# Performance work log

Measured on AMD Instinct MI355X. Metric: run time of the kernel, lower is better.

## Reference

```python
import jax, jax.numpy as jnp
import numpy as np

N = 50000
E = 400000
IN_FEATS = 256
HIDDEN = 64
HEADS = 8
CLASSES = 40
NEG_SLOPE = 0.2  # DGL GATConv default negative_slope


def setup_inputs() -> dict:
    key = jax.random.key(0)
    ks = jax.random.split(key, 12)
    features = jax.random.normal(ks[0], (N, IN_FEATS), dtype=jnp.float32)
    src = jax.random.randint(ks[1], (E,), 0, N, dtype=jnp.int32)
    dst = jax.random.randint(ks[2], (E,), 0, N, dtype=jnp.int32)
    s = 0.05
    # layer 0: in_feats -> HEADS*HIDDEN
    W1 = jax.random.normal(ks[3], (IN_FEATS, HEADS * HIDDEN), dtype=jnp.float32) * s
    al1 = jax.random.normal(ks[4], (HEADS, HIDDEN), dtype=jnp.float32) * s
    ar1 = jax.random.normal(ks[5], (HEADS, HIDDEN), dtype=jnp.float32) * s
    # layer 1: HEADS*HIDDEN -> HEADS*HIDDEN
    W2 = jax.random.normal(ks[6], (HEADS * HIDDEN, HEADS * HIDDEN), dtype=jnp.float32) * s
    al2 = jax.random.normal(ks[7], (HEADS, HIDDEN), dtype=jnp.float32) * s
    ar2 = jax.random.normal(ks[8], (HEADS, HIDDEN), dtype=jnp.float32) * s
    # layer 2: HEADS*HIDDEN -> 1*CLASSES
    W3 = jax.random.normal(ks[9], (HEADS * HIDDEN, CLASSES), dtype=jnp.float32) * s
    al3 = jax.random.normal(ks[10], (1, CLASSES), dtype=jnp.float32) * s
    ar3 = jax.random.normal(ks[11], (1, CLASSES), dtype=jnp.float32) * s
    return {"features": features, "src": src, "dst": dst,
            "W1": W1, "al1": al1, "ar1": ar1,
            "W2": W2, "al2": al2, "ar2": ar2,
            "W3": W3, "al3": al3, "ar3": ar3}


def gat_conv(h, W, al, ar, src, dst):
    """DGL GATConv (no bias, no residual, no activation, no dropout)."""
    H, D = al.shape
    feat = (h @ W).reshape(N, H, D)                      # [N,H,D]
    el = jnp.sum(feat * al[None], axis=-1)               # [N,H]
    er = jnp.sum(feat * ar[None], axis=-1)               # [N,H]
    e = jax.nn.leaky_relu(el[src] + er[dst], NEG_SLOPE)  # [E,H]
    # edge softmax over incoming edges of each dst node
    m = jax.ops.segment_max(e, dst, num_segments=N)      # [N,H]
    ex = jnp.exp(e - m[dst])                             # [E,H]
    denom = jax.ops.segment_sum(ex, dst, num_segments=N) # [N,H]
    alpha = ex / denom[dst]                              # [E,H]
    msg = alpha[:, :, None] * feat[src]                  # [E,H,D]
    out = jax.ops.segment_sum(msg, dst, num_segments=N)  # [N,H,D]
    return out.reshape(N, H * D)


def reference(features, src, dst, W1, al1, ar1, W2, al2, ar2, W3, al3, ar3):
    h = gat_conv(features, W1, al1, ar1, src, dst)  # [N, HEADS*HIDDEN]
    h = gat_conv(h, W2, al2, ar2, src, dst)         # [N, HEADS*HIDDEN]
    h = gat_conv(h, W3, al3, ar3, src, dst)         # [N, CLASSES]
    return h
```

## Files before the change

### kernel.cpp

```cpp
#include <hip/hip_runtime.h>
#include <hip/hip_bf16.h>

#define NN 50000
#define NE 400000
#define MPAD 50048
#define SLOTS 48

typedef __bf16 bf16x8_t __attribute__((ext_vector_type(8)));
typedef __bf16 bf16x4_t __attribute__((ext_vector_type(4)));
typedef float f32x4_t __attribute__((ext_vector_type(4)));

__device__ __forceinline__ float bhi(unsigned int u) {
    union { unsigned int i; float f; } v; v.i = u & 0xffff0000u; return v.f;
}
__device__ __forceinline__ float blo(unsigned int u) {
    union { unsigned int i; float f; } v; v.i = u << 16; return v.f;
}

__global__ __launch_bounds__(256) void prep_kernel(
    const float* __restrict__ W1, __hip_bfloat16* __restrict__ W1t,
    const float* __restrict__ W2, __hip_bfloat16* __restrict__ W2t,
    const float* __restrict__ W3, __hip_bfloat16* __restrict__ W3t,
    const float* __restrict__ al1, const float* __restrict__ ar1,
    const float* __restrict__ al2, const float* __restrict__ ar2,
    __hip_bfloat16* __restrict__ walr1, __hip_bfloat16* __restrict__ walr2) {
    int stride = gridDim.x * blockDim.x;
    for (int i = blockIdx.x * blockDim.x + threadIdx.x; i < 512 * 512; i += stride) {
        if (i < 512 * 256) {
            int n = i >> 8, k = i & 255;
            W1t[i] = __float2bfloat16(W1[k * 512 + n]);
        }
        {
            int n = i >> 9, k = i & 511;
            W2t[i] = __float2bfloat16(W2[k * 512 + n]);
        }
        if (i < 48 * 512) {
            int n = i >> 9, k = i & 511;
            W3t[i] = __float2bfloat16((n < 40) ? W3[k * 40 + n] : 0.f);
        }
        if (i < 16 * 256) {
            int j = i >> 8, k = i & 255;
            const float* v = (j < 8) ? (al1 + j * 64) : (ar1 + (j - 8) * 64);
            float s = 0.f;
            for (int d = 0; d < 64; ++d) s += W1[(size_t)k * 512 + (j & 7) * 64 + d] * v[d];
            walr1[(k >> 5) * 512 + j * 32 + (k & 31)] = __float2bfloat16(s);
        }
        if (i < 16 * 512) {
            int j = i >> 9, k = i & 511;
            const float* v = (j < 8) ? (al2 + j * 64) : (ar2 + (j - 8) * 64);
            float s = 0.f;
            for (int d = 0; d < 64; ++d) s += W2[(size_t)k * 512 + (j & 7) * 64 + d] * v[d];
            walr2[(k >> 5) * 512 + j * 32 + (k & 31)] = __float2bfloat16(s);
        }
    }
}

__global__ void build_kernel(const int* __restrict__ src, const int* __restrict__ dst,
                             int* __restrict__ deg, int* __restrict__ slot) {
    int e = blockIdx.x * blockDim.x + threadIdx.x;
    if (e < NE) {
        int d = dst[e];
        int p = atomicAdd(&deg[d], 1);
        if (p < SLOTS) slot[(size_t)d * SLOTS + p] = src[e];
    }
}

__device__ __forceinline__ void gld_lds16(const void* g, void* l) {
    __builtin_amdgcn_global_load_lds(
        (const __attribute__((address_space(1))) unsigned int*)g,
        (__attribute__((address_space(3))) unsigned int*)l, 16, 0, 0);
}

__global__ __launch_bounds__(256) void gemm1_fused(const float* __restrict__ A,
                                                   const __hip_bfloat16* __restrict__ Wt,
                                                   const __hip_bfloat16* __restrict__ walr,
                                                   __hip_bfloat16* __restrict__ C,
                                                   float* __restrict__ el,
                                                   float* __restrict__ er) {
    const int K = 256;
    __shared__ __align__(16) char smem[16384];
    char* smemA = smem;
    char* smemB = smem + 8192;
    const int row0 = blockIdx.x * 128;
    const int col0 = blockIdx.y * 128;
    const int w = threadIdx.x >> 6;
    const int lane = threadIdx.x & 63;
    const int quad = lane >> 4, l15 = lane & 15;
    const int wm = (w >> 1) * 64, wn = (w & 1) * 64;
    const int c0 = w * 2;
    const int srow = lane >> 2;
    const int skel = (lane & 3) * 8;
    const bool my_e = (blockIdx.y == 0) && ((w & 1) == 0);

    f32x4_t acc[4][4] = {};
    f32x4_t acce[4] = {};
    for (int k0 = 0; k0 < K; k0 += 32) {
        __syncthreads();
        {
#pragma unroll
            for (int cc = 0; cc < 2; ++cc) {
                int row = row0 + (c0 + cc) * 16 + srow;
                int rc = (row < NN) ? row : (NN - 1);
                const float* p = A + (size_t)rc * K + k0 + skel;
                float4 f0 = *reinterpret_cast<const float4*>(p);
                float4 f1 = *reinterpret_cast<const float4*>(p + 4);
                bf16x8_t h;
                h[0] = (__bf16)f0.x; h[1] = (__bf16)f0.y;
                h[2] = (__bf16)f0.z; h[3] = (__bf16)f0.w;
                h[4] = (__bf16)f1.x; h[5] = (__bf16)f1.y;
                h[6] = (__bf16)f1.z; h[7] = (__bf16)f1.w;
                *reinterpret_cast<bf16x8_t*>(smemA + (c0 + cc) * 1024 + srow * 64 +
                                             (lane & 3) * 16) = h;
            }
            const __hip_bfloat16* gB0 = Wt + (size_t)(col0 + c0 * 16 + srow) * K + k0 + skel;
            gld_lds16(gB0, smemB + c0 * 1024);
            gld_lds16(gB0 + (size_t)16 * K, smemB + (c0 + 1) * 1024);
        }
        __syncthreads();
        bf16x8_t a[4], b[4];
#pragma unroll
        for (int mi = 0; mi < 4; mi++)
            a[mi] = *reinterpret_cast<const bf16x8_t*>(smemA + (wm + mi * 16 + l15) * 64 + quad * 16);
#pragma unroll
        for (int ni = 0; ni < 4; ni++)
            b[ni] = *reinterpret_cast<const bf16x8_t*>(smemB + (wn + ni * 16 + l15) * 64 + quad * 16);
#pragma unroll
        for (int mi = 0; mi < 4; mi++)
#pragma unroll
            for (int ni = 0; ni < 4; ni++)
                acc[mi][ni] = __builtin_amdgcn_mfma_f32_16x16x32_bf16(a[mi], b[ni], acc[mi][ni], 0, 0, 0);
        if (my_e) {
            bf16x8_t b5 = *reinterpret_cast<const bf16x8_t*>(
                walr + (k0 >> 5) * 512 + l15 * 32 + quad * 8);
#pragma unroll
            for (int mi = 0; mi < 4; mi++)
                acce[mi] = __builtin_amdgcn_mfma_f32_16x16x32_bf16(a[mi], b5, acce[mi], 0, 0, 0);
        }
    }
#pragma unroll
    for (int mi = 0; mi < 4; mi++) {
#pragma unroll
        for (int ni = 0; ni < 4; ni++) {
#pragma unroll
            for (int r = 0; r < 4; r++) {
                int row = row0 + wm + mi * 16 + quad * 4 + r;
                if (row < NN)
                    C[(size_t)row * 512 + col0 + wn + ni * 16 + l15] =
                        __float2bfloat16(acc[mi][ni][r]);
            }
        }
    }
    if (my_e) {
#pragma unroll
        for (int mi = 0; mi < 4; mi++) {
#pragma unroll
            for (int r = 0; r < 4; r++) {
                int row = row0 + wm + mi * 16 + quad * 4 + r;
                if (row < NN) {
                    float v = acce[mi][r];
                    if (l15 < 8) el[row * 8 + l15] = v;
                    else er[row * 8 + l15 - 8] = v;
                }
            }
        }
    }
}

__global__ __launch_bounds__(256) void gemm_bt_fused(const __hip_bfloat16* __restrict__ A,
                                                     const __hip_bfloat16* __restrict__ Wt,
                                                     const __hip_bfloat16* __restrict__ walr,
                                                     __hip_bfloat16* __restrict__ C,
                                                     float* __restrict__ el,
                                                     float* __restrict__ er) {
    const int K = 512;
    __shared__ __align__(16) char smem[16384];
    char* smemA = smem;
    char* smemB = smem + 8192;
    const int row0 = blockIdx.x * 128;
    const int col0 = blockIdx.y * 128;
    const int w = threadIdx.x >> 6;
    const int lane = threadIdx.x & 63;
    const int quad = lane >> 4, l15 = lane & 15;
    const int wm = (w >> 1) * 64, wn = (w & 1) * 64;
    const int c0 = w * 2;
    const int srow = lane >> 2;
    const int skel = (lane & 3) * 8;
    const bool my_e = (blockIdx.y == 0) && ((w & 1) == 0);

    f32x4_t acc[4][4] = {};
    f32x4_t acce[4] = {};
    for (int k0 = 0; k0 < K; k0 += 32) {
        __syncthreads();
        {
            const __hip_bfloat16* gA0 = A + (size_t)(row0 + c0 * 16 + srow) * K + k0 + skel;
            const __hip_bfloat16* gB0 = Wt + (size_t)(col0 + c0 * 16 + srow) * K + k0 + skel;
            gld_lds16(gA0, smemA + c0 * 1024);
            gld_lds16(gA0 + (size_t)16 * K, smemA + (c0 + 1) * 1024);
            gld_lds16(gB0, smemB + c0 * 1024);
            gld_lds16(gB0 + (size_t)16 * K, smemB + (c0 + 1) * 1024);
        }
        __syncthreads();
        bf16x8_t a[4], b[4];
#pragma unroll
        for (int mi = 0; mi < 4; mi++)
            a[mi] = *reinterpret_cast<const bf16x8_t*>(smemA + (wm + mi * 16 + l15) * 64 + quad * 16);
#pragma unroll
        for (int ni = 0; ni < 4; ni++)
            b[ni] = *reinterpret_cast<const bf16x8_t*>(smemB + (wn + ni * 16 + l15) * 64 + quad * 16);
#pragma unroll
        for (int mi = 0; mi < 4; mi++)
#pragma unroll
            for (int ni = 0; ni < 4; ni++)
                acc[mi][ni] = __builtin_amdgcn_mfma_f32_16x16x32_bf16(a[mi], b[ni], acc[mi][ni], 0, 0, 0);
        if (my_e) {
            bf16x8_t b5 = *reinterpret_cast<const bf16x8_t*>(
                walr + (k0 >> 5) * 512 + l15 * 32 + quad * 8);
#pragma unroll
            for (int mi = 0; mi < 4; mi++)
                acce[mi] = __builtin_amdgcn_mfma_f32_16x16x32_bf16(a[mi], b5, acce[mi], 0, 0, 0);
        }
    }
#pragma unroll
    for (int mi = 0; mi < 4; mi++) {
#pragma unroll
        for (int ni = 0; ni < 4; ni++) {
#pragma unroll
            for (int r = 0; r < 4; r++) {
                int row = row0 + wm + mi * 16 + quad * 4 + r;
                if (row < NN)
                    C[(size_t)row * 512 + col0 + wn + ni * 16 + l15] =
                        __float2bfloat16(acc[mi][ni][r]);
            }
        }
    }
    if (my_e) {
#pragma unroll
        for (int mi = 0; mi < 4; mi++) {
#pragma unroll
            for (int r = 0; r < 4; r++) {
                int row = row0 + wm + mi * 16 + quad * 4 + r;
                if (row < NN) {
                    float v = acce[mi][r];
                    if (l15 < 8) el[row * 8 + l15] = v;
                    else er[row * 8 + l15 - 8] = v;
                }
            }
        }
    }
}

#define W3_LDSROW 520
__global__ __launch_bounds__(256) void gemm3_mfma(const __hip_bfloat16* __restrict__ A,
                                                  const __hip_bfloat16* __restrict__ W3t,
                                                  const float* __restrict__ al,
                                                  const float* __restrict__ ar,
                                                  __hip_bfloat16* __restrict__ C,
                                                  float* __restrict__ el,
                                                  float* __restrict__ er) {
    __shared__ __align__(16) __hip_bfloat16 wlds[48 * W3_LDSROW];
    for (int c = threadIdx.x; c < 48 * 64; c += 256) {
        int n = c >> 6, koff = (c & 63) * 8;
        *reinterpret_cast<uint4*>(&wlds[n * W3_LDSROW + koff]) =
            *reinterpret_cast<const uint4*>(W3t + n * 512 + koff);
    }
    __syncthreads();
    const int w = threadIdx.x >> 6;
    const int lane = threadIdx.x & 63;
    const int quad = lane >> 4, l15 = lane & 15;
    const int row0 = blockIdx.x * 64 + w * 16;

    float alv[3], arv[3];
#pragma unroll
    for (int c = 0; c < 3; c++) {
        int col = c * 16 + l15;
        alv[c] = (col < 40) ? al[col] : 0.f;
        arv[c] = (col < 40) ? ar[col] : 0.f;
    }

    f32x4_t acc[3] = {};
    const __hip_bfloat16* arow = A + (size_t)(row0 + l15) * 512;
#pragma unroll 4
    for (int k0 = 0; k0 < 512; k0 += 32) {
        bf16x8_t a = *reinterpret_cast<const bf16x8_t*>(arow + k0 + quad * 8);
#pragma unroll
        for (int c = 0; c < 3; c++) {
            bf16x8_t b = *reinterpret_cast<const bf16x8_t*>(
                &wlds[(c * 16 + l15) * W3_LDSROW + k0 + quad * 8]);
            acc[c] = __builtin_amdgcn_mfma_f32_16x16x32_bf16(a, b, acc[c], 0, 0, 0);
        }
    }
#pragma unroll
    for (int r = 0; r < 4; r++) {
        int row = row0 + quad * 4 + r;
        bool rok = row < NN;
        float pl = 0.f, pr = 0.f;
#pragma unroll
        for (int c = 0; c < 3; c++) {
            float v = acc[c][r];
            if (rok) C[(size_t)row * 64 + c * 16 + l15] = __float2bfloat16(v);
            pl += v * alv[c];
            pr += v * arv[c];
        }
        if (rok) C[(size_t)row * 64 + 48 + l15] = __float2bfloat16(0.f);
        pl += __shfl_xor(pl, 1, 64); pr += __shfl_xor(pr, 1, 64);
        pl += __shfl_xor(pl, 2, 64); pr += __shfl_xor(pr, 2, 64);
        pl += __shfl_xor(pl, 4, 64); pr += __shfl_xor(pr, 4, 64);
        pl += __shfl_xor(pl, 8, 64); pr += __shfl_xor(pr, 8, 64);
        if (l15 == 0 && rok) { el[row] = pl; er[row] = pr; }
    }
}

__global__ __launch_bounds__(256) void agg8_kernel(const __hip_bfloat16* __restrict__ feat,
                                                   const float* __restrict__ el,
                                                   const float* __restrict__ er,
                                                   const int* __restrict__ deg,
                                                   const int* __restrict__ slot,
                                                   __hip_bfloat16* __restrict__ out) {
    int gw = (blockIdx.x * blockDim.x + threadIdx.x) >> 6;
    int n = gw >> 1, w = gw & 1;
    int lane = threadIdx.x & 63;
    if (n >= NN) return;
    const int es = lane >> 2;
    const int h4 = lane & 3;
    const int hd = lane >> 4;
    int dn = min(deg[n], SLOTS);
    float er_n = er[n * 8 + w * 4 + h4];
    const int* sl = slot + (size_t)n * SLOTS;

    float lsum = 0.f;
    float acc[4] = {};
    for (int base = 0; base < dn; base += 16) {
        int e = base + es;
        bool valid = e < dn;
        int s = valid ? sl[e] : 0;
        float t = el[s * 8 + w * 4 + h4] + er_n;
        float x = (t >= 0.f) ? t : 0.2f * t;
        float p = valid ? __expf(x) : 0.f;
        lsum += p;
        int cnt = min(16, dn - base);
        for (int j = 0; j < cnt; ++j) {
            int sj = __shfl(s, j * 4, 64);
            float pj = __shfl(p, j * 4 + hd, 64);
            uint2 q = *reinterpret_cast<const uint2*>(feat + (size_t)sj * 512 + w * 256 + lane * 4);
            acc[0] += pj * blo(q.x); acc[1] += pj * bhi(q.x);
            acc[2] += pj * blo(q.y); acc[3] += pj * bhi(q.y);
        }
    }
    lsum += __shfl_xor(lsum, 4, 64);
    lsum += __shfl_xor(lsum, 8, 64);
    lsum += __shfl_xor(lsum, 16, 64);
    lsum += __shfl_xor(lsum, 32, 64);
    float lh = __shfl(lsum, hd, 64);
    float inv = (lh > 0.f) ? 1.f / lh : 0.f;
    bf16x4_t o4;
#pragma unroll
    for (int d = 0; d < 4; ++d) o4[d] = (__bf16)(acc[d] * inv);
    *reinterpret_cast<bf16x4_t*>(out + (size_t)n * 512 + w * 256 + lane * 4) = o4;
}

__global__ __launch_bounds__(256) void agg3_kernel(const __hip_bfloat16* __restrict__ feat,
                                                   const float* __restrict__ el,
                                                   const float* __restrict__ er,
                                                   const int* __restrict__ deg,
                                                   const int* __restrict__ slot,
                                                   float* __restrict__ out) {
    int n = (blockIdx.x * blockDim.x + threadIdx.x) >> 6;
    int lane = threadIdx.x & 63;
    if (n >= NN) return;
    const int es = lane >> 3;
    const int dc = lane & 7;
    int dn = min(deg[n], SLOTS);
    float er_n = er[n];
    const int* sl = slot + (size_t)n * SLOTS;

    float lsum = 0.f;
    float acc[8] = {};
    for (int base = 0; base < dn; base += 16) {
        int e0 = base + es, e1 = base + 8 + es;
        bool v0 = e0 < dn, v1 = e1 < dn;
        int s0 = v0 ? sl[e0] : 0;
        int s1 = v1 ? sl[e1] : 0;
        float t0 = el[s0] + er_n;
        float t1 = el[s1] + er_n;
        float x0 = (t0 >= 0.f) ? t0 : 0.2f * t0;
        float x1 = (t1 >= 0.f) ? t1 : 0.2f * t1;
        float p0 = v0 ? __expf(x0) : 0.f;
        float p1 = v1 ? __expf(x1) : 0.f;
        lsum += p0 + p1;
        uint4 q0 = *reinterpret_cast<const uint4*>(feat + (size_t)s0 * 64 + dc * 8);
        uint4 q1 = *reinterpret_cast<const uint4*>(feat + (size_t)s1 * 64 + dc * 8);
        acc[0] += p0 * blo(q0.x) + p1 * blo(q1.x);
        acc[1] += p0 * bhi(q0.x) + p1 * bhi(q1.x);
        acc[2] += p0 * blo(q0.y) + p1 * blo(q1.y);
        acc[3] += p0 * bhi(q0.y) + p1 * bhi(q1.y);
        acc[4] += p0 * blo(q0.z) + p1 * blo(q1.z);
        acc[5] += p0 * bhi(q0.z) + p1 * bhi(q1.z);
        acc[6] += p0 * blo(q0.w) + p1 * blo(q1.w);
        acc[7] += p0 * bhi(q0.w) + p1 * bhi(q1.w);
    }
    lsum += __shfl_xor(lsum, 8, 64);
    lsum += __shfl_xor(lsum, 16, 64);
    lsum += __shfl_xor(lsum, 32, 64);
#pragma unroll
    for (int d = 0; d < 8; ++d) {
        acc[d] += __shfl_xor(acc[d], 8, 64);
        acc[d] += __shfl_xor(acc[d], 16, 64);
        acc[d] += __shfl_xor(acc[d], 32, 64);
    }
    float inv = (lsum > 0.f) ? 1.f / lsum : 0.f;
    if (es == 0 && dc < 5) {
        float4 o0 = make_float4(acc[0] * inv, acc[1] * inv, acc[2] * inv, acc[3] * inv);
        float4 o1 = make_float4(acc[4] * inv, acc[5] * inv, acc[6] * inv, acc[7] * inv);
        *reinterpret_cast<float4*>(out + (size_t)n * 40 + dc * 8) = o0;
        *reinterpret_cast<float4*>(out + (size_t)n * 40 + dc * 8 + 4) = o1;
    }
}

extern "C" void kernel_launch(void* const* d_in, const int* in_sizes, int n_in,
                              void* d_out, int out_size, void* d_ws, size_t ws_size,
                              hipStream_t stream) {
    const float* features = (const float*)d_in[0];
    const int* src = (const int*)d_in[1];
    const int* dst = (const int*)d_in[2];
    const float* W1 = (const float*)d_in[3];
    const float* al1 = (const float*)d_in[4];
    const float* ar1 = (const float*)d_in[5];
    const float* W2 = (const float*)d_in[6];
    const float* al2 = (const float*)d_in[7];
    const float* ar2 = (const float*)d_in[8];
    const float* W3 = (const float*)d_in[9];
    const float* al3 = (const float*)d_in[10];
    const float* ar3 = (const float*)d_in[11];

    char* ws = (char*)d_ws;
    size_t o = 0;
    auto carve = [&](size_t bytes) -> void* {
        o = (o + 255) & ~(size_t)255;
        void* p = ws + o;
        o += bytes;
        return p;
    };
    __hip_bfloat16* Fbf = (__hip_bfloat16*)carve((size_t)MPAD * 512 * 2);
    __hip_bfloat16* Gbf = (__hip_bfloat16*)carve((size_t)MPAD * 512 * 2);
    __hip_bfloat16* W1t = (__hip_bfloat16*)carve((size_t)512 * 256 * 2);
    __hip_bfloat16* W2t = (__hip_bfloat16*)carve((size_t)512 * 512 * 2);
    __hip_bfloat16* W3t = (__hip_bfloat16*)carve((size_t)48 * 512 * 2);
    __hip_bfloat16* walr1 = (__hip_bfloat16*)carve((size_t)16 * 256 * 2);
    __hip_bfloat16* walr2 = (__hip_bfloat16*)carve((size_t)16 * 512 * 2);
    float* el = (float*)carve((size_t)NN * 8 * 4);
    float* er = (float*)carve((size_t)NN * 8 * 4);
    float* el3 = (float*)carve((size_t)NN * 4);
    float* er3 = (float*)carve((size_t)NN * 4);
    int* deg = (int*)carve((size_t)NN * 4);
    int* slot = (int*)carve((size_t)NN * SLOTS * 4);

    hipMemsetAsync(deg, 0, (size_t)NN * 4, stream);
    build_kernel<<<(NE + 255) / 256, 256, 0, stream>>>(src, dst, deg, slot);
    prep_kernel<<<512, 256, 0, stream>>>(W1, W1t, W2, W2t, W3, W3t,
                                         al1, ar1, al2, ar2, walr1, walr2);

    const int gmm = MPAD / 128;
    gemm1_fused<<<dim3(gmm, 4), 256, 0, stream>>>(features, W1t, walr1, Fbf, el, er);
    agg8_kernel<<<(2 * NN + 3) / 4, 256, 0, stream>>>(Fbf, el, er, deg, slot, Gbf);
    gemm_bt_fused<<<dim3(gmm, 4), 256, 0, stream>>>(Gbf, W2t, walr2, Fbf, el, er);
    agg8_kernel<<<(2 * NN + 3) / 4, 256, 0, stream>>>(Fbf, el, er, deg, slot, Gbf);
    gemm3_mfma<<<MPAD / 64, 256, 0, stream>>>(Gbf, W3t, al3, ar3, Fbf, el3, er3);
    agg3_kernel<<<(NN + 3) / 4, 256, 0, stream>>>(Fbf, el3, er3, deg, slot, (float*)d_out);
}
```

Measured before the change: 440.6 us.

## Aggregate all 8 heads per wavefront with 16-byte gathers and 4-way unrolled edges

The 8-head aggregation kernel now gives each destination node a single wavefront covering all 512 features, instead of two wavefronts each covering half. Each lane loads 8 bf16 values (16 bytes) per source row and gets the source index through readlane. The edge loop is unrolled by four so several independent gathers are in flight at once. This halves the wavefront count and the redundant slot, el and exp work per node, at the cost of more registers per lane and fewer waves to hide latency.

```diff
diff --git a/kernel.cpp b/kernel.cpp
--- a/kernel.cpp
+++ b/kernel.cpp
@@ -310,52 +310,75 @@
     }
 }
 
+__device__ __forceinline__ void fma8(float* acc, float pj, const uint4& q) {
+    acc[0] += pj * blo(q.x); acc[1] += pj * bhi(q.x);
+    acc[2] += pj * blo(q.y); acc[3] += pj * bhi(q.y);
+    acc[4] += pj * blo(q.z); acc[5] += pj * bhi(q.z);
+    acc[6] += pj * blo(q.w); acc[7] += pj * bhi(q.w);
+}
+
 __global__ __launch_bounds__(256) void agg8_kernel(const __hip_bfloat16* __restrict__ feat,
                                                    const float* __restrict__ el,
                                                    const float* __restrict__ er,
                                                    const int* __restrict__ deg,
                                                    const int* __restrict__ slot,
                                                    __hip_bfloat16* __restrict__ out) {
-    int gw = (blockIdx.x * blockDim.x + threadIdx.x) >> 6;
-    int n = gw >> 1, w = gw & 1;
+    int n = (blockIdx.x * blockDim.x + threadIdx.x) >> 6;
     int lane = threadIdx.x & 63;
     if (n >= NN) return;
-    const int es = lane >> 2;
-    const int h4 = lane & 3;
-    const int hd = lane >> 4;
+    const int es = lane >> 3;
+    const int h8 = lane & 7;
+    const int hd = lane >> 3;
     int dn = min(deg[n], SLOTS);
-    float er_n = er[n * 8 + w * 4 + h4];
+    float er_n = er[n * 8 + h8];
     const int* sl = slot + (size_t)n * SLOTS;
 
     float lsum = 0.f;
-    float acc[4] = {};
-    for (int base = 0; base < dn; base += 16) {
+    float acc[8] = {};
+    for (int base = 0; base < dn; base += 8) {
         int e = base + es;
         bool valid = e < dn;
         int s = valid ? sl[e] : 0;
-        float t = el[s * 8 + w * 4 + h4] + er_n;
+        float t = el[s * 8 + h8] + er_n;
         float x = (t >= 0.f) ? t : 0.2f * t;
         float p = valid ? __expf(x) : 0.f;
         lsum += p;
-        int cnt = min(16, dn - base);
-        for (int j = 0; j < cnt; ++j) {
-            int sj = __shfl(s, j * 4, 64);
-            float pj = __shfl(p, j * 4 + hd, 64);
-            uint2 q = *reinterpret_cast<const uint2*>(feat + (size_t)sj * 512 + w * 256 + lane * 4);
-            acc[0] += pj * blo(q.x); acc[1] += pj * bhi(q.x);
-            acc[2] += pj * blo(q.y); acc[3] += pj * bhi(q.y);
-        }
-    }
-    lsum += __shfl_xor(lsum, 4, 64);
+        int cnt = min(8, dn - base);
+        int j = 0;
+        for (; j + 4 <= cnt; j += 4) {
+            int s0 = __builtin_amdgcn_readlane(s, (j + 0) * 8);
+            int s1 = __builtin_amdgcn_readlane(s, (j + 1) * 8);
+            int s2 = __builtin_amdgcn_readlane(s, (j + 2) * 8);
+            int s3 = __builtin_amdgcn_readlane(s, (j + 3) * 8);
+            float p0 = __shfl(p, (j + 0) * 8 + hd, 64);
+            float p1 = __shfl(p, (j + 1) * 8 + hd, 64);
+            float p2 = __shfl(p, (j + 2) * 8 + hd, 64);
+            float p3 = __shfl(p, (j + 3) * 8 + hd, 64);
+            uint4 q0 = *reinterpret_cast<const uint4*>(feat + (size_t)s0 * 512 + lane * 8);
+            uint4 q1 = *reinterpret_cast<const uint4*>(feat + (size_t)s1 * 512 + lane * 8);
+            uint4 q2 = *reinterpret_cast<const uint4*>(feat + (size_t)s2 * 512 + lane * 8);
+            uint4 q3 = *reinterpret_cast<const uint4*>(feat + (size_t)s3 * 512 + lane * 8);
+            fma8(acc, p0, q0);
+            fma8(acc, p1, q1);
+            fma8(acc, p2, q2);
+            fma8(acc, p3, q3);
+        }
+        for (; j < cnt; ++j) {
+            int sj = __builtin_amdgcn_readlane(s, j * 8);
+            float pj = __shfl(p, j * 8 + hd, 64);
+            uint4 q = *reinterpret_cast<const uint4*>(feat + (size_t)sj * 512 + lane * 8);
+            fma8(acc, pj, q);
+        }
+    }
     lsum += __shfl_xor(lsum, 8, 64);
     lsum += __shfl_xor(lsum, 16, 64);
     lsum += __shfl_xor(lsum, 32, 64);
     float lh = __shfl(lsum, hd, 64);
     float inv = (lh > 0.f) ? 1.f / lh : 0.f;
-    bf16x4_t o4;
-#pragma unroll
-    for (int d = 0; d < 4; ++d) o4[d] = (__bf16)(acc[d] * inv);
-    *reinterpret_cast<bf16x4_t*>(out + (size_t)n * 512 + w * 256 + lane * 4) = o4;
+    bf16x8_t o8;
+#pragma unroll
+    for (int d = 0; d < 8; ++d) o8[d] = (__bf16)(acc[d] * inv);
+    *reinterpret_cast<bf16x8_t*>(out + (size_t)n * 512 + lane * 8) = o8;
 }
 
 __global__ __launch_bounds__(256) void agg3_kernel(const __hip_bfloat16* __restrict__ feat,
@@ -461,9 +484,9 @@
 
     const int gmm = MPAD / 128;
     gemm1_fused<<<dim3(gmm, 4), 256, 0, stream>>>(features, W1t, walr1, Fbf, el, er);
-    agg8_kernel<<<(2 * NN + 3) / 4, 256, 0, stream>>>(Fbf, el, er, deg, slot, Gbf);
+    agg8_kernel<<<(NN + 3) / 4, 256, 0, stream>>>(Fbf, el, er, deg, slot, Gbf);
     gemm_bt_fused<<<dim3(gmm, 4), 256, 0, stream>>>(Gbf, W2t, walr2, Fbf, el, er);
-    agg8_kernel<<<(2 * NN + 3) / 4, 256, 0, stream>>>(Fbf, el, er, deg, slot, Gbf);
+    agg8_kernel<<<(NN + 3) / 4, 256, 0, stream>>>(Fbf, el, er, deg, slot, Gbf);
     gemm3_mfma<<<MPAD / 64, 256, 0, stream>>>(Gbf, W3t, al3, ar3, Fbf, el3, er3);
     agg3_kernel<<<(NN + 3) / 4, 256, 0, stream>>>(Fbf, el3, er3, deg, slot, (float*)d_out);
 }
```

Measured after the change: 425.1 us. -3.5%, faster.
